# Performance work log

Hardware: AMD Instinct MI355X
Metric: run time of the kernel (lower is better)

Reference implementation:

```python
import jax, jax.numpy as jnp
import numpy as np

D_MODEL = 1024
NUM_HEADS = 16
ROPE_THETA = 10000.0


def _rope(v, pos, theta=ROPE_THETA):
    # v: [B, S, D] (full d_model, as in the original module), pos: [B, S] int
    d = v.shape[-1]
    inv_freq = theta ** (-jnp.arange(0, d, 2, dtype=jnp.float32) / d)  # [D/2]
    ang = pos.astype(jnp.float32)[..., None] * inv_freq  # [B, S, D/2]
    cos, sin = jnp.cos(ang), jnp.sin(ang)
    x1, x2 = v[..., ::2], v[..., 1::2]
    r1 = x1 * cos - x2 * sin
    r2 = x1 * sin + x2 * cos
    return jnp.stack([r1, r2], axis=-1).reshape(v.shape)


def setup_inputs() -> dict:
    key = jax.random.key(0)
    ks = jax.random.split(key, 6)
    B, S, D = 2, 2048, D_MODEL
    std = np.sqrt(2.0 / (D + D)).astype(np.float32)
    x = jax.random.normal(ks[0], (B, S, D), dtype=jnp.float32)
    token_positions = jnp.sort(jax.random.randint(ks[1], (B, S), 0, S), axis=-1).astype(jnp.int32)
    wq = jax.random.normal(ks[2], (D, D), dtype=jnp.float32) * std
    wk = jax.random.normal(ks[3], (D, D), dtype=jnp.float32) * std
    wv = jax.random.normal(ks[4], (D, D), dtype=jnp.float32) * std
    wo = jax.random.normal(ks[5], (D, D), dtype=jnp.float32) * std
    return {"x": x, "token_positions": token_positions, "wq": wq, "wk": wk, "wv": wv, "wo": wo}


def reference(x, token_positions, wq, wk, wv, wo):
    B, S, D = x.shape
    H = NUM_HEADS
    dk = D // H
    # Projections (nn.functional.linear: x @ W^T)
    q = x @ wq.T
    k = x @ wk.T
    v = x @ wv.T
    # In the original, Q/K are reshaped to heads and back before RoPE -> identity;
    # RoPE is applied over the FULL d_model dimension.
    q = _rope(q, token_positions)
    k = _rope(k, token_positions)
    # Split heads
    q = q.reshape(B, S, H, dk)
    k = k.reshape(B, S, H, dk)
    v = v.reshape(B, S, H, dk)
    scores = jnp.einsum('bqhd,bkhd->bhqk', q, k) / jnp.sqrt(jnp.asarray(dk, x.dtype))
    causal = jnp.tril(jnp.ones((S, S), dtype=bool))  # True where allowed
    scores = jnp.where(causal[None, None], scores, -jnp.inf)
    attn = jax.nn.softmax(scores, axis=-1)
    out = jnp.einsum('bhqk,bkhd->bqhd', attn, v).reshape(B, S, D)
    return out @ wo.T
```

## Files before the change

### kernel.cpp

```cpp
#include <hip/hip_runtime.h>
#include <hip/hip_bf16.h>
#include <math.h>

typedef __attribute__((ext_vector_type(8))) short bf16x8;
typedef __attribute__((ext_vector_type(4))) short short4x;
typedef __attribute__((ext_vector_type(4))) float f32x4;
typedef __attribute__((ext_vector_type(8))) float f32x8;

#define D_MODEL 1024
#define NHEADS  16
#define DK      64
#define BATCH   2
#define SEQ     2048

static __device__ __forceinline__ short f2bf(float f) {
    unsigned u = __builtin_bit_cast(unsigned, f);
    u = u + 0x7FFFu + ((u >> 16) & 1u);
    return (short)(u >> 16);
}
static __device__ __forceinline__ short f2bf_fast(float f) {
    return (short)((__builtin_bit_cast(unsigned, f) + 0x8000u) >> 16);
}
static __device__ __forceinline__ float bf2f(short s) {
    return __builtin_bit_cast(float, ((unsigned)(unsigned short)s) << 16);
}

typedef __attribute__((address_space(3))) unsigned int lds_uint;
typedef __attribute__((address_space(1))) const unsigned int glob_uint;
static __device__ __forceinline__ void gl2lds16(const short* g, short* l) {
    __builtin_amdgcn_global_load_lds((glob_uint*)g, (lds_uint*)l, 16, 0, 0);
}

#define NX8 ((BATCH * SEQ * D_MODEL) / 8)
#define NW8 ((D_MODEL * D_MODEL) / 8)
__global__ void cvt_all_kernel(const void* __restrict__ x,  const void* __restrict__ wq,
                               const void* __restrict__ wk, const void* __restrict__ wv,
                               const void* __restrict__ wo,
                               __hip_bfloat16* __restrict__ xb,  __hip_bfloat16* __restrict__ wqb,
                               __hip_bfloat16* __restrict__ wkb, __hip_bfloat16* __restrict__ wvb,
                               __hip_bfloat16* __restrict__ wob,
                               int* __restrict__ dtf)
{
    __shared__ int sflag;
    if (threadIdx.x < 64) {
        const unsigned w = ((const unsigned*)x)[threadIdx.x];
        const unsigned e = (w >> 7) & 0xFFu;
        const bool weird = (e >= 0x88u) || (e <= 0x5Fu);
        const unsigned long long m = __ballot(weird);
        if (threadIdx.x == 0) {
            const int f = (__popcll(m) >= 16) ? 1 : 0;
            sflag = f;
            if (blockIdx.x == 0) *dtf = f;
        }
    }
    __syncthreads();

    const int i = blockIdx.x * blockDim.x + threadIdx.x;
    if (i >= NX8 + 4 * NW8) return;
    const void* src; __hip_bfloat16* dst; int off;
    if (i < NX8) { src = x; dst = xb; off = i; }
    else {
        const int j = i - NX8, seg = j >> 17; off = j & (NW8 - 1);
        switch (seg) {
            case 0: src = wq; dst = wqb; break;
            case 1: src = wk; dst = wkb; break;
            case 2: src = wv; dst = wvb; break;
            default: src = wo; dst = wob; break;
        }
    }
    if (sflag) {
        const f32x8 v = ((const f32x8*)src)[off];
        bf16x8 r;
#pragma unroll
        for (int j = 0; j < 8; ++j) r[j] = f2bf(v[j]);
        ((bf16x8*)dst)[off] = r;
    } else {
        ((bf16x8*)dst)[off] = ((const bf16x8*)src)[off];
    }
}

static __device__ __forceinline__ void gemm128_main(
    const short* __restrict__ A, const short* __restrict__ B,
    int K, int bm, int bn, f32x4 (&acc)[4][4], short* lds)
{
    const int tid  = threadIdx.x;
    const int lane = tid & 63;
    const int wave = tid >> 6;
    const int l16  = lane & 15;
    const int quad = lane >> 4;

    const int srow = lane >> 2;
    const int scg  = (lane & 3) ^ ((lane >> 3) & 3);
    const short* ag = A + (size_t)(bm + wave * 32 + srow) * K + scg * 8;
    const short* bg = B + (size_t)(bn + wave * 32 + srow) * K + scg * 8;
    const int dst = wave * 1024 + lane * 8;

    const int mrow = (wave >> 1) * 64;
    const int nrow = (wave & 1) * 64;
    const int ph   = ((quad ^ ((l16 >> 1) & 3))) * 8;

    auto stage = [&](int k0, int buf) {
        short* ad = lds + buf * 4096 + dst;
        short* bd = lds + 8192 + buf * 4096 + dst;
        gl2lds16(ag + k0, ad);
        gl2lds16(ag + k0 + (size_t)16 * K, ad + 512);
        gl2lds16(bg + k0, bd);
        gl2lds16(bg + k0 + (size_t)16 * K, bd + 512);
    };

    stage(0, 0);
    for (int k0 = 0, t = 0; k0 < K; k0 += 32, ++t) {
        __asm__ volatile("s_waitcnt vmcnt(0)" ::: "memory");
        __syncthreads();
        if (k0 + 32 < K) stage(k0 + 32, (t + 1) & 1);

        const short* Ab = lds + (t & 1) * 4096;
        const short* Bb = lds + 8192 + (t & 1) * 4096;
        bf16x8 a[4], b[4];
#pragma unroll
        for (int x = 0; x < 4; ++x)
            a[x] = *(const bf16x8*)(Ab + (mrow + x * 16 + l16) * 32 + ph);
#pragma unroll
        for (int y = 0; y < 4; ++y)
            b[y] = *(const bf16x8*)(Bb + (nrow + y * 16 + l16) * 32 + ph);
#pragma unroll
        for (int x = 0; x < 4; ++x)
#pragma unroll
            for (int y = 0; y < 4; ++y)
                acc[x][y] = __builtin_amdgcn_mfma_f32_16x16x32_bf16(
                    a[x], b[y], acc[x][y], 0, 0, 0);
    }
}

__global__ __launch_bounds__(256) void gemm_qkv_kernel(
    const __hip_bfloat16* __restrict__ xb,
    const __hip_bfloat16* __restrict__ wqb,
    const __hip_bfloat16* __restrict__ wkb,
    const __hip_bfloat16* __restrict__ wvb,
    const int* __restrict__ pos,
    __hip_bfloat16* __restrict__ Qb,
    __hip_bfloat16* __restrict__ Kb,
    __hip_bfloat16* __restrict__ Vt)
{
    __shared__ alignas(16) short lds[16384];
    const int wsel = blockIdx.x >> 3;
    const int bn   = (blockIdx.x & 7) * 128;
    const int bm   = blockIdx.y * 128;
    const short* W = (const short*)(wsel == 0 ? wqb : (wsel == 1 ? wkb : wvb));

    f32x4 acc[4][4];
#pragma unroll
    for (int x = 0; x < 4; ++x)
#pragma unroll
        for (int y = 0; y < 4; ++y) acc[x][y] = (f32x4){0.f, 0.f, 0.f, 0.f};

    gemm128_main((const short*)xb, W, D_MODEL, bm, bn, acc, lds);

    const int lane = threadIdx.x & 63;
    const int wave = threadIdx.x >> 6;
    const int l16  = lane & 15;
    const int quad = lane >> 4;

    if (wsel == 2) {
#pragma unroll
        for (int x = 0; x < 4; ++x)
#pragma unroll
            for (int y = 0; y < 4; ++y)
#pragma unroll
                for (int r = 0; r < 4; ++r) {
                    const int row = bm + (wave >> 1) * 64 + x * 16 + quad * 4 + r;
                    const int col = bn + (wave & 1) * 64 + y * 16 + l16;
                    const int hh = col >> 6, dcol = col & 63;
                    const int bb = row >> 11, ss = row & (SEQ - 1);
                    Vt[(((size_t)bb * NHEADS + hh) * DK + dcol) * SEQ + ss] =
                        __float2bfloat16(acc[x][y][r]);
                }
        return;
    }

    __hip_bfloat16* Crm = (wsel == 1) ? Kb : Qb;
    const float qscale = (wsel == 0) ? 0.125f : 1.0f;
#pragma unroll
    for (int x = 0; x < 4; ++x)
#pragma unroll
        for (int r = 0; r < 4; ++r) {
            const int row = bm + (wave >> 1) * 64 + x * 16 + quad * 4 + r;
            const float p = (float)pos[row];
#pragma unroll
            for (int y = 0; y < 4; ++y) {
                const int col = bn + (wave & 1) * 64 + y * 16 + l16;
                const float inv = exp2f((float)(col >> 1) * -0.02595256257f);
                const float ang = p * inv;
                const float c = __cosf(ang), s = __sinf(ang);
                const float v  = acc[x][y][r];
                const float pv = __shfl_xor(v, 1);
                const float vr = v * c + pv * ((l16 & 1) ? s : -s);
                Crm[(size_t)row * D_MODEL + col] = __float2bfloat16(vr * qscale);
            }
        }
}

__global__ __launch_bounds__(256) void gemm_out_kernel(
    const __hip_bfloat16* __restrict__ AO,
    const __hip_bfloat16* __restrict__ wob,
    void* __restrict__ C, const int* __restrict__ dtf)
{
    __shared__ alignas(16) short lds[2][6144];
    const int tid  = threadIdx.x;
    const int lane = tid & 63;
    const int wave = tid >> 6;
    const int l16  = lane & 15;
    const int quad = lane >> 4;
    const int bn = blockIdx.x * 128;
    const int bm = blockIdx.y * 64;
    const bool c32 = (*dtf) != 0;
    const int K = D_MODEL;

    const int srow = lane >> 2;
    const int scg  = (lane & 3) ^ ((lane >> 3) & 3);
    const short* Ap = (const short*)AO;
    const short* Bp = (const short*)wob;
    const short* ag = Ap + (size_t)(bm + wave * 16 + srow) * K + scg * 8;
    const short* bg = Bp + (size_t)(bn + wave * 32 + srow) * K + scg * 8;

    const int nrow = wave * 32;
    const int ph   = ((quad ^ ((l16 >> 1) & 3))) * 8;

    f32x4 acc[4][2];
#pragma unroll
    for (int x = 0; x < 4; ++x)
#pragma unroll
        for (int y = 0; y < 2; ++y) acc[x][y] = (f32x4){0.f, 0.f, 0.f, 0.f};

    auto stage = [&](int k0, int buf) {
        gl2lds16(ag + k0, &lds[buf][wave * 512 + lane * 8]);
        gl2lds16(bg + k0, &lds[buf][2048 + wave * 1024 + lane * 8]);
        gl2lds16(bg + k0 + (size_t)16 * K, &lds[buf][2048 + wave * 1024 + 512 + lane * 8]);
    };

    stage(0, 0);
    for (int k0 = 0, t = 0; k0 < K; k0 += 32, ++t) {
        __asm__ volatile("s_waitcnt vmcnt(0)" ::: "memory");
        __syncthreads();
        if (k0 + 32 < K) stage(k0 + 32, (t + 1) & 1);

        const short* Ab = &lds[t & 1][0];
        const short* Bb = &lds[t & 1][2048];
        bf16x8 a[4], b[2];
#pragma unroll
        for (int x = 0; x < 4; ++x)
            a[x] = *(const bf16x8*)(Ab + (x * 16 + l16) * 32 + ph);
#pragma unroll
        for (int y = 0; y < 2; ++y)
            b[y] = *(const bf16x8*)(Bb + (nrow + y * 16 + l16) * 32 + ph);
#pragma unroll
        for (int x = 0; x < 4; ++x)
#pragma unroll
            for (int y = 0; y < 2; ++y)
                acc[x][y] = __builtin_amdgcn_mfma_f32_16x16x32_bf16(
                    a[x], b[y], acc[x][y], 0, 0, 0);
    }

#pragma unroll
    for (int x = 0; x < 4; ++x)
#pragma unroll
        for (int y = 0; y < 2; ++y)
#pragma unroll
            for (int r = 0; r < 4; ++r) {
                const int row = bm + x * 16 + quad * 4 + r;
                const int col = bn + nrow + y * 16 + l16;
                const size_t idx = (size_t)row * D_MODEL + col;
                if (c32) ((float*)C)[idx] = acc[x][y][r];
                else     ((__hip_bfloat16*)C)[idx] = __float2bfloat16(acc[x][y][r]);
            }
}

__global__ __launch_bounds__(256, 2) void flash_attn_kernel(
    __hip_bfloat16* QO,
    const __hip_bfloat16* __restrict__ Kt,
    const __hip_bfloat16* __restrict__ Vt)
{
    __shared__ alignas(16) char pool[66560];
    short* k_lds = (short*)pool;
    short* v_lds = (short*)(pool + 32768);

    const int lane = threadIdx.x & 63;
    const int wave = threadIdx.x >> 6;
    const int l16  = lane & 15;
    const int quad = lane >> 4;
    const int qt   = 31 - blockIdx.y;
    const int bh   = blockIdx.x;
    const int b    = bh >> 4;
    const int h    = bh & 15;
    const size_t base  = (size_t)b * SEQ * D_MODEL + h * DK;
    const size_t vbase = (size_t)bh * DK * SEQ;

    const short* Qp = (const short*)QO;
    const short* Kp = (const short*)Kt;
    const short* Vp = (const short*)Vt;

    bf16x8 aq[4][2];
#pragma unroll
    for (int qf = 0; qf < 4; ++qf)
#pragma unroll
        for (int ks = 0; ks < 2; ++ks)
            aq[qf][ks] = *(const bf16x8*)(Qp + base +
                (size_t)(qt * 64 + qf * 16 + l16) * D_MODEL + ks * 32 + quad * 8);

    f32x4 o[4][4];
    float ls[4] = {0.f, 0.f, 0.f, 0.f};
#pragma unroll
    for (int qf = 0; qf < 4; ++qf)
#pragma unroll
        for (int nf = 0; nf < 4; ++nf) o[qf][nf] = (f32x4){0.f, 0.f, 0.f, 0.f};

    const int srow = lane >> 3;
    const int scg  = (lane & 7) ^ srow;
    const short* kg = Kp + ((size_t)b * SEQ + wave * 32 + srow) * D_MODEL + h * DK + scg * 8;
    const int ge = (l16 & 8) | ((l16 & 7) ^ quad);
    const int go = (l16 & 8) | ((l16 & 7) ^ (4 + quad));
    const short* vgA = Vp + vbase + (size_t)(wave * 16 + quad) * SEQ + ge * 8;
    const short* vgB = Vp + vbase + (size_t)(wave * 16 + 4 + quad) * SEQ + go * 8;

    auto stage = [&](int t, int buf) {
        const int kv0 = t * 128;
        short* kd = k_lds + buf * 8192 + (wave * 32) * 64 + lane * 8;
#pragma unroll
        for (int i = 0; i < 4; ++i)
            gl2lds16(kg + (size_t)(kv0 + i * 8) * D_MODEL, kd + i * 8 * 64);
        short* vd = v_lds + buf * 8192 + (wave * 16) * 128 + lane * 8;
        gl2lds16(vgA + kv0,                 vd);
        gl2lds16(vgB + kv0,                 vd + 4 * 128);
        gl2lds16(vgA + (size_t)8 * SEQ + kv0, vd + 8 * 128);
        gl2lds16(vgB + (size_t)8 * SEQ + kv0, vd + 12 * 128);
    };

    auto compute = [&](int buf, int kv0, bool tail) {
        const short* kb = k_lds + buf * 8192;
        const short* vb = v_lds + buf * 8192;
        bf16x8 ak[2][2];
#pragma unroll
        for (int kvf = 0; kvf < 2; ++kvf)
#pragma unroll
            for (int ks = 0; ks < 2; ++ks) {
                const int row = wave * 32 + kvf * 16 + l16;
                const int g = (ks * 4 + quad) ^ (l16 & 7);
                ak[kvf][ks] = *(const bf16x8*)(kb + row * 64 + g * 8);
            }
        f32x4 s[2][4];
        __builtin_amdgcn_s_setprio(1);
#pragma unroll
        for (int kvf = 0; kvf < 2; ++kvf)
#pragma unroll
            for (int qf = 0; qf < 4; ++qf) {
                f32x4 c = (f32x4){0.f, 0.f, 0.f, 0.f};
                c = __builtin_amdgcn_mfma_f32_16x16x32_bf16(ak[kvf][0], aq[qf][0], c, 0, 0, 0);
                c = __builtin_amdgcn_mfma_f32_16x16x32_bf16(ak[kvf][1], aq[qf][1], c, 0, 0, 0);
                s[kvf][qf] = c;
            }
        __builtin_amdgcn_s_setprio(0);

        bf16x8 pa[4];
#pragma unroll
        for (int qf = 0; qf < 4; ++qf) {
            const int qrow = qt * 64 + qf * 16 + l16;
#pragma unroll
            for (int kvf = 0; kvf < 2; ++kvf)
#pragma unroll
                for (int r = 0; r < 4; ++r) {
                    float p = __expf(s[kvf][qf][r]);
                    if (tail && (kv0 + wave * 32 + kvf * 16 + quad * 4 + r > qrow))
                        p = 0.f;
                    ls[qf] += p;
                    pa[qf][kvf * 4 + r] = f2bf_fast(p);
                }
        }

        if (tail) { __asm__ volatile("s_waitcnt vmcnt(0)" ::: "memory"); }
        else      { __asm__ volatile("s_waitcnt vmcnt(8)" ::: "memory"); }
        __builtin_amdgcn_s_barrier();

        bf16x8 bv[4];
#pragma unroll
        for (int nf = 0; nf < 4; ++nf) {
            const int d = nf * 16 + l16;
#pragma unroll
            for (int e = 0; e < 2; ++e) {
                const int g  = wave * 4 + e * 2 + (quad >> 1);
                const int gs = (g & 8) | ((g & 7) ^ (l16 & 7));
                const short4x v4 = *(const short4x*)(vb + d * 128 + gs * 8 + (quad & 1) * 4);
                bv[nf][e * 4 + 0] = v4[0];
                bv[nf][e * 4 + 1] = v4[1];
                bv[nf][e * 4 + 2] = v4[2];
                bv[nf][e * 4 + 3] = v4[3];
            }
        }
        __builtin_amdgcn_s_setprio(1);
#pragma unroll
        for (int qf = 0; qf < 4; ++qf)
#pragma unroll
            for (int nf = 0; nf < 4; ++nf)
                o[qf][nf] = __builtin_amdgcn_mfma_f32_16x16x32_bf16(
                    pa[qf], bv[nf], o[qf][nf], 0, 0, 0);
        __builtin_amdgcn_s_setprio(0);
    };

    const int tmax = qt >> 1;
    stage(0, 0);
    for (int t = 0; t < tmax; ++t) {
        __asm__ volatile("s_waitcnt vmcnt(4)" ::: "memory");
        __builtin_amdgcn_s_barrier();
        stage(t + 1, (t + 1) & 1);
        compute(t & 1, t * 128, false);
    }
    __asm__ volatile("s_waitcnt vmcnt(4)" ::: "memory");
    __builtin_amdgcn_s_barrier();
    compute(tmax & 1, tmax * 128, true);

#pragma unroll
    for (int qf = 0; qf < 4; ++qf) {
        ls[qf] += __shfl_xor(ls[qf], 16);
        ls[qf] += __shfl_xor(ls[qf], 32);
    }
    __syncthreads();
    float* red = (float*)pool;
    float* lsb = (float*)(pool + 65536);
#pragma unroll
    for (int qf = 0; qf < 4; ++qf)
#pragma unroll
        for (int nf = 0; nf < 4; ++nf)
            *(f32x4*)(red + ((wave * 16 + qf * 4 + nf) * 64 + lane) * 4) = o[qf][nf];
    if (quad == 0)
#pragma unroll
        for (int qf = 0; qf < 4; ++qf) lsb[wave * 64 + qf * 16 + l16] = ls[qf];
    __syncthreads();

    f32x4 lden = (f32x4){0.f, 0.f, 0.f, 0.f};
#pragma unroll
    for (int w = 0; w < 4; ++w)
        lden += *(const f32x4*)(lsb + w * 64 + wave * 16 + quad * 4);
    f32x4 osum[4];
#pragma unroll
    for (int nf = 0; nf < 4; ++nf) {
        f32x4 a = (f32x4){0.f, 0.f, 0.f, 0.f};
#pragma unroll
        for (int w = 0; w < 4; ++w)
            a += *(const f32x4*)(red + ((w * 16 + wave * 4 + nf) * 64 + lane) * 4);
        osum[nf] = a;
    }
    float inv[4];
#pragma unroll
    for (int r = 0; r < 4; ++r) inv[r] = 1.f / fmaxf(lden[r], 1e-20f);
#pragma unroll
    for (int nf = 0; nf < 4; ++nf)
#pragma unroll
        for (int r = 0; r < 4; ++r)
            QO[base + (size_t)(qt * 64 + wave * 16 + quad * 4 + r) * D_MODEL
                    + nf * 16 + l16]
                = __float2bfloat16(osum[nf][r] * inv[r]);
}

extern "C" void kernel_launch(void* const* d_in, const int* in_sizes, int n_in,
                              void* d_out, int out_size, void* d_ws, size_t ws_size,
                              hipStream_t stream)
{
    (void)in_sizes; (void)n_in; (void)out_size; (void)ws_size;

    const void* x  = d_in[0];
    const int*  pos = (const int*)d_in[1];
    const void* wq = d_in[2];
    const void* wk = d_in[3];
    const void* wv = d_in[4];
    const void* wo = d_in[5];

    const int M = BATCH * SEQ;
    const int D = D_MODEL;
    const size_t MD = (size_t)M * D;
    const size_t DD = (size_t)D * D;

    int* dtf = (int*)d_ws;
    __hip_bfloat16* xb  = (__hip_bfloat16*)((char*)d_ws + 256);
    __hip_bfloat16* wqb = xb  + MD;
    __hip_bfloat16* wkb = wqb + DD;
    __hip_bfloat16* wvb = wkb + DD;
    __hip_bfloat16* wob = wvb + DD;
    __hip_bfloat16* Qb  = wob + DD;
    __hip_bfloat16* Vtb = Qb  + MD;
    __hip_bfloat16* Kb  = (__hip_bfloat16*)d_out;

    dim3 blk(256);

    const int ncvt = NX8 + 4 * NW8;
    hipLaunchKernelGGL(cvt_all_kernel, dim3((ncvt + 255) / 256), blk, 0, stream,
                       x, wq, wk, wv, wo, xb, wqb, wkb, wvb, wob, dtf);

    hipLaunchKernelGGL(gemm_qkv_kernel, dim3(24, 32), blk, 0, stream,
                       xb, wqb, wkb, wvb, pos, Qb, Kb, Vtb);

    hipLaunchKernelGGL(flash_attn_kernel, dim3(32, 32), blk, 0, stream,
                       Qb, Kb, Vtb);

    hipLaunchKernelGGL(gemm_out_kernel, dim3(D / 128, M / 64), blk, 0, stream,
                       Qb, wob, d_out, dtf);
}
```

Measured before the change: 173.1 us.

## Double GEMM K-tile to 64 with 8-way XOR swizzle; fold log2e into Q scale

The shared 128x128 GEMM main loop now stages 64-wide K slices instead of 32. It uses an 8-chunk XOR-swizzled LDS layout and issues two MFMA sub-steps per barrier, so the number of sync/wait iterations is halved. LDS per block doubles to 64 KB, which may reduce occupancy. Separately, log2(e) is folded into the Q scale so attention can use a raw exp2 builtin instead of __expf, saving a multiply per probability element.

Measured after the change: 174.9 us. Within noise of the previous version (+1.0%).

```diff
diff --git a/kernel.cpp b/kernel.cpp
--- a/kernel.cpp
+++ b/kernel.cpp
@@ -12,6 +12,12 @@
 #define DK      64
 #define BATCH   2
 #define SEQ     2048
+
+#if __has_builtin(__builtin_amdgcn_exp2f)
+#define EXP2(x) __builtin_amdgcn_exp2f(x)
+#else
+#define EXP2(x) exp2f(x)
+#endif
 
 static __device__ __forceinline__ short f2bf(float f) {
     unsigned u = __builtin_bit_cast(unsigned, f);
@@ -89,46 +95,50 @@
     const int l16  = lane & 15;
     const int quad = lane >> 4;
 
-    const int srow = lane >> 2;
-    const int scg  = (lane & 3) ^ ((lane >> 3) & 3);
+    const int srow = lane >> 3;
+    const int scg  = (lane & 7) ^ srow;
     const short* ag = A + (size_t)(bm + wave * 32 + srow) * K + scg * 8;
     const short* bg = B + (size_t)(bn + wave * 32 + srow) * K + scg * 8;
-    const int dst = wave * 1024 + lane * 8;
 
     const int mrow = (wave >> 1) * 64;
     const int nrow = (wave & 1) * 64;
-    const int ph   = ((quad ^ ((l16 >> 1) & 3))) * 8;
 
     auto stage = [&](int k0, int buf) {
-        short* ad = lds + buf * 4096 + dst;
-        short* bd = lds + 8192 + buf * 4096 + dst;
-        gl2lds16(ag + k0, ad);
-        gl2lds16(ag + k0 + (size_t)16 * K, ad + 512);
-        gl2lds16(bg + k0, bd);
-        gl2lds16(bg + k0 + (size_t)16 * K, bd + 512);
+        short* ab = lds + buf * 16384 + (wave * 32) * 64 + lane * 8;
+        short* bb = ab + 8192;
+#pragma unroll
+        for (int i = 0; i < 4; ++i)
+            gl2lds16(ag + (size_t)(i * 8) * K + k0, ab + i * 8 * 64);
+#pragma unroll
+        for (int i = 0; i < 4; ++i)
+            gl2lds16(bg + (size_t)(i * 8) * K + k0, bb + i * 8 * 64);
     };
 
     stage(0, 0);
-    for (int k0 = 0, t = 0; k0 < K; k0 += 32, ++t) {
+    for (int k0 = 0, t = 0; k0 < K; k0 += 64, ++t) {
         __asm__ volatile("s_waitcnt vmcnt(0)" ::: "memory");
         __syncthreads();
-        if (k0 + 32 < K) stage(k0 + 32, (t + 1) & 1);
-
-        const short* Ab = lds + (t & 1) * 4096;
-        const short* Bb = lds + 8192 + (t & 1) * 4096;
-        bf16x8 a[4], b[4];
-#pragma unroll
-        for (int x = 0; x < 4; ++x)
-            a[x] = *(const bf16x8*)(Ab + (mrow + x * 16 + l16) * 32 + ph);
-#pragma unroll
-        for (int y = 0; y < 4; ++y)
-            b[y] = *(const bf16x8*)(Bb + (nrow + y * 16 + l16) * 32 + ph);
-#pragma unroll
-        for (int x = 0; x < 4; ++x)
+        if (k0 + 64 < K) stage(k0 + 64, (t + 1) & 1);
+
+        const short* Ab = lds + (t & 1) * 16384;
+        const short* Bb = Ab + 8192;
+#pragma unroll
+        for (int ks = 0; ks < 2; ++ks) {
+            bf16x8 a[4], b[4];
+            const int g = ((ks * 4 + quad) ^ (l16 & 7)) * 8;
+#pragma unroll
+            for (int x = 0; x < 4; ++x)
+                a[x] = *(const bf16x8*)(Ab + (mrow + x * 16 + l16) * 64 + g);
 #pragma unroll
             for (int y = 0; y < 4; ++y)
-                acc[x][y] = __builtin_amdgcn_mfma_f32_16x16x32_bf16(
-                    a[x], b[y], acc[x][y], 0, 0, 0);
+                b[y] = *(const bf16x8*)(Bb + (nrow + y * 16 + l16) * 64 + g);
+#pragma unroll
+            for (int x = 0; x < 4; ++x)
+#pragma unroll
+                for (int y = 0; y < 4; ++y)
+                    acc[x][y] = __builtin_amdgcn_mfma_f32_16x16x32_bf16(
+                        a[x], b[y], acc[x][y], 0, 0, 0);
+        }
     }
 }
 
@@ -142,7 +152,7 @@
     __hip_bfloat16* __restrict__ Kb,
     __hip_bfloat16* __restrict__ Vt)
 {
-    __shared__ alignas(16) short lds[16384];
+    __shared__ alignas(16) short lds[32768];
     const int wsel = blockIdx.x >> 3;
     const int bn   = (blockIdx.x & 7) * 128;
     const int bm   = blockIdx.y * 128;
@@ -179,7 +189,7 @@
     }
 
     __hip_bfloat16* Crm = (wsel == 1) ? Kb : Qb;
-    const float qscale = (wsel == 0) ? 0.125f : 1.0f;
+    const float qscale = (wsel == 0) ? 0.18033688011f : 1.0f;
 #pragma unroll
     for (int x = 0; x < 4; ++x)
 #pragma unroll
@@ -368,7 +378,7 @@
             for (int kvf = 0; kvf < 2; ++kvf)
 #pragma unroll
                 for (int r = 0; r < 4; ++r) {
-                    float p = __expf(s[kvf][qf][r]);
+                    float p = EXP2(s[kvf][qf][r]);
                     if (tail && (kv0 + wave * 32 + kvf * 16 + quad * 4 + r > qrow))
                         p = 0.f;
                     ls[qf] += p;
```
